# Performance work log

Measured on AMD Instinct MI355X. Metric: run time of the kernel, lower is better.

The kernel has to match this reference:

```python
import jax, jax.numpy as jnp
import numpy as np

B, C, H, W = 8, 512, 64, 64
HEADS, GROUPS, EPS = 4, 32, 1e-5


def setup_inputs() -> dict:
    key = jax.random.key(0)
    ks = jax.random.split(key, 7)
    s = 0.02
    return {
        "x": jax.random.normal(ks[0], (B, C, H, W), dtype=jnp.float32),
        "gn_w": jnp.ones((C,), dtype=jnp.float32),
        "gn_b": jnp.zeros((C,), dtype=jnp.float32),
        "qkv_w": jax.random.normal(ks[1], (3 * C, C), dtype=jnp.float32) * s,
        "qkv_b": jnp.zeros((3 * C,), dtype=jnp.float32),
        "proj_w": jax.random.normal(ks[2], (C, C), dtype=jnp.float32) * s,
        "proj_b": jnp.zeros((C,), dtype=jnp.float32),
    }


def reference(x, gn_w, gn_b, qkv_w, qkv_b, proj_w, proj_b):
    b, c, h, w = x.shape
    d = c // HEADS  # per-head channel dim
    n = h * w
    # GroupNorm(32, C)
    xg = x.reshape(b, GROUPS, -1)
    mu = xg.mean(axis=-1, keepdims=True)
    var = xg.var(axis=-1, keepdims=True)
    hn = ((xg - mu) * jax.lax.rsqrt(var + EPS)).reshape(b, c, h, w)
    hn = hn * gn_w[:, None, None] + gn_b[:, None, None]
    # 1x1 conv qkv: [3C, C] contraction over channels
    qkv = jnp.einsum('oc,bchw->bohw', qkv_w, hn) + qkv_b[:, None, None]
    qkv = qkv.reshape(b, 3, HEADS, d, n)
    q, k, v = qkv[:, 0], qkv[:, 1], qkv[:, 2]  # each [b, heads, d, n]
    # NOTE: as in the source, q @ k^T contracts over spatial dim -> [b,heads,d,d]
    attn = jnp.einsum('bhdn,bhen->bhde', q, k) * (d ** -0.5)
    attn = jax.nn.softmax(attn, axis=-1)
    out = jnp.einsum('bhde,bhen->bhdn', attn, v).reshape(b, c, h, w)
    out = jnp.einsum('oc,bchw->bohw', proj_w, out) + proj_b[:, None, None]
    return x + out
```

## Files before the change

### kernel.cpp

```cpp
#include <hip/hip_runtime.h>
#include <hip/hip_bf16.h>

typedef __hip_bfloat16 bf16;
typedef __bf16 v8bf __attribute__((ext_vector_type(8)));
typedef float  v4f  __attribute__((ext_vector_type(4)));

struct __align__(8) bf16x4 { bf16 x, y, z, w; };

__device__ __forceinline__ bf16 f2b(float v) { return __float2bfloat16(v); }

#define NSP 4096
#define CCH 512

__device__ __forceinline__ void async_cp16(const bf16* g, __bf16* l) {
    __builtin_amdgcn_global_load_lds(
        (const __attribute__((address_space(1))) unsigned int*)(unsigned long long)g,
        (__attribute__((address_space(3))) unsigned int*)(unsigned int)(unsigned long long)l,
        16, 0, 0);
}

__global__ __launch_bounds__(256) void wconv_kernel(const float* __restrict__ src,
                                                    bf16* __restrict__ dst, int n4) {
    int i = blockIdx.x * 256 + threadIdx.x;
    if (i < n4) {
        float4 v = ((const float4*)src)[i];
        bf16x4 o = { f2b(v.x), f2b(v.y), f2b(v.z), f2b(v.w) };
        ((bf16x4*)dst)[i] = o;
    }
}

__global__ __launch_bounds__(256) void gn_stats_kernel(const float* __restrict__ x,
                                                       float* __restrict__ stats) {
    int blk = blockIdx.x;
    int b = blk >> 5, g = blk & 31;
    size_t base = ((size_t)(b * CCH + g * 16)) * NSP;
    const float4* xp4 = (const float4*)(x + base);
    int t = threadIdx.x;
    float s = 0.f, s2 = 0.f;
    for (int i = t; i < 16384; i += 256) {
        float4 v = xp4[i];
        s  += v.x + v.y + v.z + v.w;
        s2 += v.x * v.x + v.y * v.y + v.z * v.z + v.w * v.w;
    }
    for (int off = 32; off > 0; off >>= 1) {
        s  += __shfl_down(s, off);
        s2 += __shfl_down(s2, off);
    }
    __shared__ float red[8];
    int wid = t >> 6, lid = t & 63;
    if (lid == 0) { red[wid] = s; red[wid + 4] = s2; }
    __syncthreads();
    if (t == 0) {
        float ts  = red[0] + red[1] + red[2] + red[3];
        float ts2 = red[4] + red[5] + red[6] + red[7];
        float mean = ts * (1.f / 65536.f);
        float var  = ts2 * (1.f / 65536.f) - mean * mean;
        stats[blk * 2]     = mean;
        stats[blk * 2 + 1] = rsqrtf(var + 1e-5f);
    }
}

__global__ __launch_bounds__(256) void gn_norm_t_kernel(const float* __restrict__ x,
                                                        const float* __restrict__ gw,
                                                        const float* __restrict__ gb,
                                                        const float* __restrict__ stats,
                                                        bf16* __restrict__ hnT) {
    __shared__ float sT[64][65];
    int n0 = blockIdx.x * 64, c0 = blockIdx.y * 64, b = blockIdx.z;
    int t = threadIdx.x;
    int cl = t >> 4, nl4 = (t & 15) << 2;
#pragma unroll
    for (int it = 0; it < 4; ++it) {
        int crow = cl + it * 16;
        int c = c0 + crow;
        int bg = b * 32 + (c >> 4);
        float mean = stats[bg * 2], rstd = stats[bg * 2 + 1];
        float wsc = gw[c] * rstd;
        float bb  = gb[c] - mean * wsc;
        float4 v = *(const float4*)&x[((long)b * CCH + c) * NSP + n0 + nl4];
        sT[crow][nl4 + 0] = v.x * wsc + bb;
        sT[crow][nl4 + 1] = v.y * wsc + bb;
        sT[crow][nl4 + 2] = v.z * wsc + bb;
        sT[crow][nl4 + 3] = v.w * wsc + bb;
    }
    __syncthreads();
    int nl = t >> 4, cl4 = (t & 15) << 2;
#pragma unroll
    for (int it = 0; it < 4; ++it) {
        int nrow = nl + it * 16;
        bf16x4 ov = { f2b(sT[cl4 + 0][nrow]), f2b(sT[cl4 + 1][nrow]),
                      f2b(sT[cl4 + 2][nrow]), f2b(sT[cl4 + 3][nrow]) };
        *(bf16x4*)&hnT[((long)b * NSP + n0 + nrow) * CCH + c0 + cl4] = ov;
    }
}

__device__ __forceinline__ void gemm_core(const bf16* __restrict__ A, long as,
                                          const bf16* __restrict__ B, long bs,
                                          int K, v4f acc[4][4],
                                          __bf16* sA, __bf16* sB) {
    int t = threadIdx.x;
    int lane = t & 63, wv = t >> 6;
    int wr = wv >> 1, wc = wv & 1;
    int lq = lane & 15, quad = lane >> 4;
    int r0 = wv * 16 + (lane >> 2);
    int koff = (lane & 3) * 8;
    __bf16* ldsA0 = sA + wv * 512 + lane * 8;
    __bf16* ldsA1 = ldsA0 + 2048;
    __bf16* ldsB0 = sB + wv * 512 + lane * 8;
    __bf16* ldsB1 = ldsB0 + 2048;
    const __bf16* aBase = sA + (wr * 64) * 32;
    const __bf16* bBase = sB + (wc * 64) * 32;

    for (int k0 = 0; k0 < K; k0 += 32) {
        __syncthreads();
        async_cp16(A + (long)r0 * as + k0 + koff,        ldsA0);
        async_cp16(A + (long)(r0 + 64) * as + k0 + koff, ldsA1);
        async_cp16(B + (long)r0 * bs + k0 + koff,        ldsB0);
        async_cp16(B + (long)(r0 + 64) * bs + k0 + koff, ldsB1);
        __syncthreads();
        v8bf a[4], bf[4];
#pragma unroll
        for (int i = 0; i < 4; ++i)
            a[i] = *(const v8bf*)(aBase + (i * 16 + lq) * 32 + quad * 8);
#pragma unroll
        for (int j = 0; j < 4; ++j)
            bf[j] = *(const v8bf*)(bBase + (j * 16 + lq) * 32 + quad * 8);
#pragma unroll
        for (int i = 0; i < 4; ++i)
#pragma unroll
            for (int j = 0; j < 4; ++j)
                acc[i][j] = __builtin_amdgcn_mfma_f32_16x16x32_bf16(a[i], bf[j], acc[i][j], 0, 0, 0);
    }
}

__global__ __launch_bounds__(256) void qkv_gemm_kernel(const bf16* __restrict__ hnT,
                                                       const bf16* __restrict__ qkv_wb,
                                                       const float* __restrict__ qkv_b,
                                                       bf16* __restrict__ qkbuf,
                                                       bf16* __restrict__ vT) {
    __shared__ __align__(16) __bf16 sA[128 * 32];
    __shared__ __align__(16) __bf16 sB[128 * 32];
    int n0 = blockIdx.x * 128, o0 = blockIdx.y * 128, b = blockIdx.z;
    v4f acc[4][4] = {};
    gemm_core(hnT + ((long)b * NSP + n0) * CCH, CCH,
              qkv_wb + (long)o0 * CCH, CCH, CCH, acc, sA, sB);
    int t = threadIdx.x, lane = t & 63, wv = t >> 6, wr = wv >> 1, wc = wv & 1;
    int lq = lane & 15, quad = lane >> 4;
#pragma unroll
    for (int j = 0; j < 4; ++j) {
        int o = o0 + wc * 64 + j * 16 + lq;
        float bias = qkv_b[o];
#pragma unroll
        for (int i = 0; i < 4; ++i) {
            int n = n0 + wr * 64 + i * 16 + quad * 4;
            v4f v = acc[i][j];
            if (o0 < 1024) {
                bf16x4 ov = { f2b(v[0] + bias), f2b(v[1] + bias),
                              f2b(v[2] + bias), f2b(v[3] + bias) };
                *(bf16x4*)&qkbuf[((long)b * 1024 + o) * NSP + n] = ov;
            } else {
#pragma unroll
                for (int r = 0; r < 4; ++r)
                    vT[((long)b * NSP + n + r) * CCH + (o - 1024)] = f2b(v[r] + bias);
            }
        }
    }
}

__global__ __launch_bounds__(256) void qk_gemm_kernel(const bf16* __restrict__ qkbuf,
                                                      float* __restrict__ P_part) {
    __shared__ __align__(16) __bf16 sA[128 * 32];
    __shared__ __align__(16) __bf16 sB[128 * 32];
    int s = blockIdx.x, bh = blockIdx.y;
    int b = bh >> 2, h = bh & 3;
    const bf16* q  = qkbuf + ((long)b * 1024 + h * 128) * NSP + s * 512;
    const bf16* kk = qkbuf + ((long)b * 1024 + 512 + h * 128) * NSP + s * 512;
    v4f acc[4][4] = {};
    gemm_core(q, NSP, kk, NSP, 512, acc, sA, sB);
    float* Pp = P_part + ((long)s * 32 + bh) * 16384;
    int t = threadIdx.x, lane = t & 63, wv = t >> 6, wr = wv >> 1, wc = wv & 1;
    int lq = lane & 15, quad = lane >> 4;
#pragma unroll
    for (int j = 0; j < 4; ++j) {
        int e = wc * 64 + j * 16 + lq;
#pragma unroll
        for (int i = 0; i < 4; ++i) {
            int d = wr * 64 + i * 16 + quad * 4;
            v4f v = acc[i][j];
#pragma unroll
            for (int r = 0; r < 4; ++r) Pp[(long)(d + r) * 128 + e] = v[r];
        }
    }
}

__global__ __launch_bounds__(128) void softmax_kernel(const float* __restrict__ P_part,
                                                      bf16* __restrict__ Pb) {
    int row = blockIdx.x;
    int bh = row >> 7, d = row & 127;
    int t = threadIdx.x;
    float v = 0.f;
#pragma unroll
    for (int s = 0; s < 8; ++s)
        v += P_part[((long)s * 32 + bh) * 16384 + (long)d * 128 + t];
    v *= 0.08838834764831845f;
    float m = v;
    for (int off = 32; off > 0; off >>= 1) m = fmaxf(m, __shfl_down(m, off));
    __shared__ float sm[2];
    if ((t & 63) == 0) sm[t >> 6] = m;
    __syncthreads();
    m = fmaxf(sm[0], sm[1]);
    float e = __expf(v - m);
    float ssum = e;
    for (int off = 32; off > 0; off >>= 1) ssum += __shfl_down(ssum, off);
    __shared__ float ss[2];
    if ((t & 63) == 0) ss[t >> 6] = ssum;
    __syncthreads();
    ssum = ss[0] + ss[1];
    Pb[(long)row * 128 + t] = f2b(e / ssum);
}

__global__ __launch_bounds__(256) void pv_gemm_kernel(const bf16* __restrict__ Pb,
                                                      const bf16* __restrict__ vT,
                                                      bf16* __restrict__ attT) {
    __shared__ __align__(16) __bf16 sA[128 * 32];
    __shared__ __align__(16) __bf16 sB[128 * 32];
    int n0 = blockIdx.x * 128, bh = blockIdx.y;
    int b = bh >> 2, h = bh & 3;
    v4f acc[4][4] = {};
    gemm_core(Pb + (long)bh * 16384, 128,
              vT + ((long)b * NSP + n0) * CCH + h * 128, CCH, 128, acc, sA, sB);
    int t = threadIdx.x, lane = t & 63, wv = t >> 6, wr = wv >> 1, wc = wv & 1;
    int lq = lane & 15, quad = lane >> 4;
#pragma unroll
    for (int j = 0; j < 4; ++j) {
        int n = n0 + wc * 64 + j * 16 + lq;
#pragma unroll
        for (int i = 0; i < 4; ++i) {
            int d = wr * 64 + i * 16 + quad * 4;
            v4f v = acc[i][j];
            bf16x4 ov = { f2b(v[0]), f2b(v[1]), f2b(v[2]), f2b(v[3]) };
            *(bf16x4*)&attT[((long)b * NSP + n) * CCH + h * 128 + d] = ov;
        }
    }
}

__global__ __launch_bounds__(256) void proj_gemm_kernel(const bf16* __restrict__ attT,
                                                        const bf16* __restrict__ proj_wb,
                                                        const float* __restrict__ proj_b,
                                                        const float* __restrict__ x,
                                                        float* __restrict__ out) {
    __shared__ __align__(16) __bf16 sA[128 * 32];
    __shared__ __align__(16) __bf16 sB[128 * 32];
    int n0 = blockIdx.x * 128, c0 = blockIdx.y * 128, b = blockIdx.z;
    v4f acc[4][4] = {};
    gemm_core(attT + ((long)b * NSP + n0) * CCH, CCH,
              proj_wb + (long)c0 * CCH, CCH, CCH, acc, sA, sB);
    int t = threadIdx.x, lane = t & 63, wv = t >> 6, wr = wv >> 1, wc = wv & 1;
    int lq = lane & 15, quad = lane >> 4;
#pragma unroll
    for (int j = 0; j < 4; ++j) {
        int c = c0 + wc * 64 + j * 16 + lq;
        float bias = proj_b[c];
#pragma unroll
        for (int i = 0; i < 4; ++i) {
            int n = n0 + wr * 64 + i * 16 + quad * 4;
            long idx = ((long)b * CCH + c) * NSP + n;
            float4 r = *(const float4*)&x[idx];
            v4f v = acc[i][j];
            float4 ov = { v[0] + bias + r.x, v[1] + bias + r.y,
                          v[2] + bias + r.z, v[3] + bias + r.w };
            *(float4*)&out[idx] = ov;
        }
    }
}

extern "C" void kernel_launch(void* const* d_in, const int* in_sizes, int n_in,
                              void* d_out, int out_size, void* d_ws, size_t ws_size,
                              hipStream_t stream) {
    const float* x      = (const float*)d_in[0];
    const float* gn_w   = (const float*)d_in[1];
    const float* gn_b   = (const float*)d_in[2];
    const float* qkv_w  = (const float*)d_in[3];
    const float* qkv_b  = (const float*)d_in[4];
    const float* proj_w = (const float*)d_in[5];
    const float* proj_b = (const float*)d_in[6];
    float* out = (float*)d_out;

    char* ws = (char*)d_ws;
    bf16*  hnT    = (bf16*)ws;
    float* P_part = (float*)ws;
    bf16*  attT   = (bf16*)ws;
    bf16*  qkbuf  = (bf16*)(ws + 33554432);
    bf16*  vT     = (bf16*)(ws + 100663296);
    bf16*  Pb     = (bf16*)(ws + 134217728);
    float* stats  = (float*)(ws + 135266304);
    bf16*  qkv_wb = (bf16*)(ws + 135270400);
    bf16*  proj_wb= (bf16*)(ws + 136843264);

    wconv_kernel<<<768, 256, 0, stream>>>(qkv_w, qkv_wb, 196608);
    wconv_kernel<<<256, 256, 0, stream>>>(proj_w, proj_wb, 65536);
    gn_stats_kernel<<<256, 256, 0, stream>>>(x, stats);
    gn_norm_t_kernel<<<dim3(64, 8, 8), 256, 0, stream>>>(x, gn_w, gn_b, stats, hnT);
    qkv_gemm_kernel<<<dim3(32, 12, 8), 256, 0, stream>>>(hnT, qkv_wb, qkv_b, qkbuf, vT);
    qk_gemm_kernel<<<dim3(8, 32), 256, 0, stream>>>(qkbuf, P_part);
    softmax_kernel<<<4096, 128, 0, stream>>>(P_part, Pb);
    pv_gemm_kernel<<<dim3(32, 32), 256, 0, stream>>>(Pb, vT, attT);
    proj_gemm_kernel<<<dim3(32, 4, 8), 256, 0, stream>>>(attT, proj_wb, proj_b, x, out);
}
```

Before: 318.6 us.

## Use 256x256 double-buffered LDS GEMM core for qkv and proj projections

Replaces the 128x128 single-stage GEMM used by the qkv and proj 1x1-conv kernels with a 256x256 tile, 512-thread core. It uses 128KB of LDS double-buffering with 64-wide K tiles, XOR-swizzled addresses, async global-to-LDS loads staged between MFMA phases, and s_setprio around the MFMA bursts. The goal is more operand reuse per tile and overlap of memory traffic with compute. In exchange there are fewer blocks (768 and 256), higher register and LDS pressure that limits occupancy, and a hand-tuned vmcnt schedule that is fragile to compiler changes.

After: 305.5 us. 4.1% less time.

```diff
diff --git a/kernel.cpp b/kernel.cpp
--- a/kernel.cpp
+++ b/kernel.cpp
@@ -133,35 +133,176 @@
     }
 }
 
-__global__ __launch_bounds__(256) void qkv_gemm_kernel(const bf16* __restrict__ hnT,
-                                                       const bf16* __restrict__ qkv_wb,
-                                                       const float* __restrict__ qkv_b,
-                                                       bf16* __restrict__ qkbuf,
-                                                       bf16* __restrict__ vT) {
-    __shared__ __align__(16) __bf16 sA[128 * 32];
-    __shared__ __align__(16) __bf16 sB[128 * 32];
-    int n0 = blockIdx.x * 128, o0 = blockIdx.y * 128, b = blockIdx.z;
-    v4f acc[4][4] = {};
-    gemm_core(hnT + ((long)b * NSP + n0) * CCH, CCH,
-              qkv_wb + (long)o0 * CCH, CCH, CCH, acc, sA, sB);
-    int t = threadIdx.x, lane = t & 63, wv = t >> 6, wr = wv >> 1, wc = wv & 1;
+__device__ __forceinline__ void gemm256_core(const bf16* __restrict__ A, long lda,
+                                             const bf16* __restrict__ B, long ldb,
+                                             int K, v4f acc[8][4], char* sLds) {
+    const int t = threadIdx.x;
+    const int lane = t & 63, wv = t >> 6;
+    const int wm = wv >> 2, wn = wv & 3;
+    const int lq = lane & 15, quad = lane >> 4;
+    const int xsw = (lq & 7) << 4;
+    const int kq0 = ((quad << 4)) ^ xsw;
+    const int kq1 = (64 | (quad << 4)) ^ xsw;
+    const int aRow0 = (wm * 128 + lq) << 7;
+    const int bRow0 = (wn * 64 + lq) << 7;
+    const int NT = K >> 6;
+
+    auto STAGE = [&](const bf16* mb, long ld, int ldsbyte, int ktile, int h) {
+#pragma unroll
+        for (int s = 0; s < 2; ++s) {
+            int L = (s << 13) + (t << 4);
+            int row = L >> 7;
+            int kb = (L & 127) ^ ((row & 7) << 4);
+            const char* g = (const char*)(mb + (long)(h * 128 + row) * ld + (long)ktile * 64);
+            async_cp16((const bf16*)(g + kb),
+                       (__bf16*)(sLds + ldsbyte + (h << 14) + L));
+        }
+    };
+
+    STAGE(B, ldb, 32768, 0, 0);
+    STAGE(B, ldb, 32768, 0, 1);
+    STAGE(A, lda, 0,     0, 0);
+    STAGE(A, lda, 0,     0, 1);
+    if (NT > 1) {
+        STAGE(B, ldb, 65536 + 32768, 1, 0);
+        STAGE(B, ldb, 65536 + 32768, 1, 1);
+        asm volatile("s_waitcnt vmcnt(4)" ::: "memory");
+    } else {
+        asm volatile("s_waitcnt vmcnt(0)" ::: "memory");
+    }
+    __builtin_amdgcn_s_barrier();
+    asm volatile("" ::: "memory");
+
+    for (int kt = 0; kt < NT; ++kt) {
+        const int cb = (kt & 1) << 16;
+        const int nb = cb ^ 65536;
+        const int bufA = cb, bufB = cb | 32768;
+        v8bf a[4][2], b0[2][2], b1[2][2];
+
+#pragma unroll
+        for (int ii = 0; ii < 4; ++ii) {
+            a[ii][0] = *(const v8bf*)(sLds + bufA + aRow0 + ((ii * 16) << 7) + kq0);
+            a[ii][1] = *(const v8bf*)(sLds + bufA + aRow0 + ((ii * 16) << 7) + kq1);
+        }
+#pragma unroll
+        for (int jj = 0; jj < 2; ++jj) {
+            b0[jj][0] = *(const v8bf*)(sLds + bufB + bRow0 + ((jj * 16) << 7) + kq0);
+            b0[jj][1] = *(const v8bf*)(sLds + bufB + bRow0 + ((jj * 16) << 7) + kq1);
+        }
+        if (kt + 1 < NT) STAGE(A, lda, nb, kt + 1, 0);
+        __builtin_amdgcn_s_barrier();
+        asm volatile("s_waitcnt lgkmcnt(0)" ::: "memory");
+        __builtin_amdgcn_sched_barrier(0);
+        __builtin_amdgcn_s_setprio(1);
+#pragma unroll
+        for (int ii = 0; ii < 4; ++ii)
+#pragma unroll
+            for (int jj = 0; jj < 2; ++jj) {
+                acc[ii][jj] = __builtin_amdgcn_mfma_f32_16x16x32_bf16(a[ii][0], b0[jj][0], acc[ii][jj], 0, 0, 0);
+                acc[ii][jj] = __builtin_amdgcn_mfma_f32_16x16x32_bf16(a[ii][1], b0[jj][1], acc[ii][jj], 0, 0, 0);
+            }
+        __builtin_amdgcn_s_setprio(0);
+        __builtin_amdgcn_s_barrier();
+        asm volatile("" ::: "memory");
+
+#pragma unroll
+        for (int jj = 0; jj < 2; ++jj) {
+            b1[jj][0] = *(const v8bf*)(sLds + bufB + bRow0 + ((32 + jj * 16) << 7) + kq0);
+            b1[jj][1] = *(const v8bf*)(sLds + bufB + bRow0 + ((32 + jj * 16) << 7) + kq1);
+        }
+        if (kt + 1 < NT) STAGE(A, lda, nb, kt + 1, 1);
+        __builtin_amdgcn_s_barrier();
+        asm volatile("s_waitcnt lgkmcnt(0)" ::: "memory");
+        __builtin_amdgcn_sched_barrier(0);
+        __builtin_amdgcn_s_setprio(1);
+#pragma unroll
+        for (int ii = 0; ii < 4; ++ii)
+#pragma unroll
+            for (int jj = 0; jj < 2; ++jj) {
+                acc[ii][2 + jj] = __builtin_amdgcn_mfma_f32_16x16x32_bf16(a[ii][0], b1[jj][0], acc[ii][2 + jj], 0, 0, 0);
+                acc[ii][2 + jj] = __builtin_amdgcn_mfma_f32_16x16x32_bf16(a[ii][1], b1[jj][1], acc[ii][2 + jj], 0, 0, 0);
+            }
+        __builtin_amdgcn_s_setprio(0);
+        __builtin_amdgcn_s_barrier();
+        asm volatile("" ::: "memory");
+
+#pragma unroll
+        for (int ii = 0; ii < 4; ++ii) {
+            a[ii][0] = *(const v8bf*)(sLds + bufA + aRow0 + ((64 + ii * 16) << 7) + kq0);
+            a[ii][1] = *(const v8bf*)(sLds + bufA + aRow0 + ((64 + ii * 16) << 7) + kq1);
+        }
+        if (kt + 2 < NT) STAGE(B, ldb, bufB, kt + 2, 0);
+        __builtin_amdgcn_s_barrier();
+        asm volatile("s_waitcnt lgkmcnt(0)" ::: "memory");
+        __builtin_amdgcn_sched_barrier(0);
+        __builtin_amdgcn_s_setprio(1);
+#pragma unroll
+        for (int ii = 0; ii < 4; ++ii)
+#pragma unroll
+            for (int jj = 0; jj < 2; ++jj) {
+                acc[4 + ii][2 + jj] = __builtin_amdgcn_mfma_f32_16x16x32_bf16(a[ii][0], b1[jj][0], acc[4 + ii][2 + jj], 0, 0, 0);
+                acc[4 + ii][2 + jj] = __builtin_amdgcn_mfma_f32_16x16x32_bf16(a[ii][1], b1[jj][1], acc[4 + ii][2 + jj], 0, 0, 0);
+            }
+        __builtin_amdgcn_s_setprio(0);
+        __builtin_amdgcn_s_barrier();
+        asm volatile("" ::: "memory");
+
+        if (kt + 2 < NT) STAGE(B, ldb, bufB, kt + 2, 1);
+        __builtin_amdgcn_s_barrier();
+        __builtin_amdgcn_s_setprio(1);
+#pragma unroll
+        for (int ii = 0; ii < 4; ++ii)
+#pragma unroll
+            for (int jj = 0; jj < 2; ++jj) {
+                acc[4 + ii][jj] = __builtin_amdgcn_mfma_f32_16x16x32_bf16(a[ii][0], b0[jj][0], acc[4 + ii][jj], 0, 0, 0);
+                acc[4 + ii][jj] = __builtin_amdgcn_mfma_f32_16x16x32_bf16(a[ii][1], b0[jj][1], acc[4 + ii][jj], 0, 0, 0);
+            }
+        __builtin_amdgcn_s_setprio(0);
+        if (kt + 2 < NT) asm volatile("s_waitcnt vmcnt(4)" ::: "memory");
+        else             asm volatile("s_waitcnt vmcnt(0)" ::: "memory");
+        __builtin_amdgcn_s_barrier();
+        asm volatile("" ::: "memory");
+    }
+}
+
+__global__ __launch_bounds__(512, 2) void qkv_gemm_kernel(const bf16* __restrict__ hnT,
+                                                          const bf16* __restrict__ qkv_wb,
+                                                          const float* __restrict__ qkv_b,
+                                                          bf16* __restrict__ qkbuf,
+                                                          bf16* __restrict__ vT) {
+    __shared__ __align__(16) char sLds[131072];
+    int n0 = blockIdx.x * 256, o0 = blockIdx.y * 256, b = blockIdx.z;
+    v4f acc[8][4] = {};
+    gemm256_core(hnT + ((long)b * NSP + n0) * CCH, CCH,
+                 qkv_wb + (long)o0 * CCH, CCH, CCH, acc, sLds);
+    int t = threadIdx.x, lane = t & 63, wv = t >> 6, wm = wv >> 2, wn = wv & 3;
     int lq = lane & 15, quad = lane >> 4;
-#pragma unroll
-    for (int j = 0; j < 4; ++j) {
-        int o = o0 + wc * 64 + j * 16 + lq;
-        float bias = qkv_b[o];
-#pragma unroll
-        for (int i = 0; i < 4; ++i) {
-            int n = n0 + wr * 64 + i * 16 + quad * 4;
-            v4f v = acc[i][j];
-            if (o0 < 1024) {
+    if (o0 < 1024) {
+#pragma unroll
+        for (int j = 0; j < 4; ++j) {
+            int o = o0 + wn * 64 + j * 16 + lq;
+            float bias = qkv_b[o];
+#pragma unroll
+            for (int i = 0; i < 8; ++i) {
+                int n = n0 + wm * 128 + i * 16 + quad * 4;
+                v4f v = acc[i][j];
                 bf16x4 ov = { f2b(v[0] + bias), f2b(v[1] + bias),
                               f2b(v[2] + bias), f2b(v[3] + bias) };
                 *(bf16x4*)&qkbuf[((long)b * 1024 + o) * NSP + n] = ov;
-            } else {
+            }
+        }
+    } else {
+#pragma unroll
+        for (int j = 0; j < 4; ++j) {
+            int e = o0 - 1024 + wn * 64 + j * 16 + lq;
+            float bias = qkv_b[1024 + e];
+#pragma unroll
+            for (int i = 0; i < 8; ++i) {
+                int n = n0 + wm * 128 + i * 16 + quad * 4;
+                v4f v = acc[i][j];
 #pragma unroll
                 for (int r = 0; r < 4; ++r)
-                    vT[((long)b * NSP + n + r) * CCH + (o - 1024)] = f2b(v[r] + bias);
+                    vT[((long)b * NSP + n + r) * CCH + e] = f2b(v[r] + bias);
             }
         }
     }
@@ -244,26 +385,25 @@
     }
 }
 
-__global__ __launch_bounds__(256) void proj_gemm_kernel(const bf16* __restrict__ attT,
-                                                        const bf16* __restrict__ proj_wb,
-                                                        const float* __restrict__ proj_b,
-                                                        const float* __restrict__ x,
-                                                        float* __restrict__ out) {
-    __shared__ __align__(16) __bf16 sA[128 * 32];
-    __shared__ __align__(16) __bf16 sB[128 * 32];
-    int n0 = blockIdx.x * 128, c0 = blockIdx.y * 128, b = blockIdx.z;
-    v4f acc[4][4] = {};
-    gemm_core(attT + ((long)b * NSP + n0) * CCH, CCH,
-              proj_wb + (long)c0 * CCH, CCH, CCH, acc, sA, sB);
-    int t = threadIdx.x, lane = t & 63, wv = t >> 6, wr = wv >> 1, wc = wv & 1;
+__global__ __launch_bounds__(512, 2) void proj_gemm_kernel(const bf16* __restrict__ attT,
+                                                           const bf16* __restrict__ proj_wb,
+                                                           const float* __restrict__ proj_b,
+                                                           const float* __restrict__ x,
+                                                           float* __restrict__ out) {
+    __shared__ __align__(16) char sLds[131072];
+    int n0 = blockIdx.x * 256, c0 = blockIdx.y * 256, b = blockIdx.z;
+    v4f acc[8][4] = {};
+    gemm256_core(attT + ((long)b * NSP + n0) * CCH, CCH,
+                 proj_wb + (long)c0 * CCH, CCH, CCH, acc, sLds);
+    int t = threadIdx.x, lane = t & 63, wv = t >> 6, wm = wv >> 2, wn = wv & 3;
     int lq = lane & 15, quad = lane >> 4;
 #pragma unroll
     for (int j = 0; j < 4; ++j) {
-        int c = c0 + wc * 64 + j * 16 + lq;
+        int c = c0 + wn * 64 + j * 16 + lq;
         float bias = proj_b[c];
 #pragma unroll
-        for (int i = 0; i < 4; ++i) {
-            int n = n0 + wr * 64 + i * 16 + quad * 4;
+        for (int i = 0; i < 8; ++i) {
+            int n = n0 + wm * 128 + i * 16 + quad * 4;
             long idx = ((long)b * CCH + c) * NSP + n;
             float4 r = *(const float4*)&x[idx];
             v4f v = acc[i][j];
@@ -301,9 +441,9 @@
     wconv_kernel<<<256, 256, 0, stream>>>(proj_w, proj_wb, 65536);
     gn_stats_kernel<<<256, 256, 0, stream>>>(x, stats);
     gn_norm_t_kernel<<<dim3(64, 8, 8), 256, 0, stream>>>(x, gn_w, gn_b, stats, hnT);
-    qkv_gemm_kernel<<<dim3(32, 12, 8), 256, 0, stream>>>(hnT, qkv_wb, qkv_b, qkbuf, vT);
+    qkv_gemm_kernel<<<dim3(16, 6, 8), 512, 0, stream>>>(hnT, qkv_wb, qkv_b, qkbuf, vT);
     qk_gemm_kernel<<<dim3(8, 32), 256, 0, stream>>>(qkbuf, P_part);
     softmax_kernel<<<4096, 128, 0, stream>>>(P_part, Pb);
     pv_gemm_kernel<<<dim3(32, 32), 256, 0, stream>>>(Pb, vT, attT);
-    proj_gemm_kernel<<<dim3(32, 4, 8), 256, 0, stream>>>(attT, proj_wb, proj_b, x, out);
-}
+    proj_gemm_kernel<<<dim3(16, 2, 8), 512, 0, stream>>>(attT, proj_wb, proj_b, x, out);
+}
```
